# Kernel tuning notes

Hardware: AMD Instinct MI355X
Metric: run time of the kernel (lower is better)

## Reference

```python
import jax, jax.numpy as jnp
import numpy as np

# (C,H,W) of x0..x11; flattened size +1 homogeneous coordinate per key
SHAPES = [(3,32,32),(96,32,32),(96,32,32),(96,16,16),(192,16,16),(192,16,16),(192,8,8),(192,8,8),(192,8,8),(640,1,1),(100,1,1),(10,1,1)]
# (Cin,Cout,k,stride,pad) for conv1..conv9
CONV = [(3,96,3,1,1),(96,96,3,1,1),(96,96,3,2,1),(96,192,3,1,1),(192,192,3,1,1),(192,192,3,2,1),(192,192,3,1,1),(192,192,1,1,0),(192,10,1,1,0)]
B = 128


def setup_inputs():
    key = jax.random.key(0)
    inp = {}
    k, key = jax.random.split(key)
    inp['x0'] = jax.random.normal(k, (int(np.prod(SHAPES[0])) + 1, B), jnp.float32)
    for i, s in enumerate(SHAPES):
        n = int(np.prod(s)) + 1
        k1, k2, key = jax.random.split(key, 3)
        inp['perm%d' % i] = jax.random.permutation(k1, n)
        inp['diag%d' % i] = jax.random.uniform(k2, (n,), jnp.float32, 0.5, 1.5)
    for j, (ci, co, ks, st, pd) in enumerate(CONV):
        k1, k2, key = jax.random.split(key, 3)
        inp['w%d' % (j + 1)] = jax.random.normal(k1, (co, ci, ks, ks), jnp.float32) / np.float32(np.sqrt(ci * ks * ks))
        inp['b%d' % (j + 1)] = jax.random.normal(k2, (co,), jnp.float32) * 0.01
    k1, k2, k3, k4 = jax.random.split(key, 4)
    inp['fw1'] = jax.random.normal(k1, (100, 640), jnp.float32) / np.float32(np.sqrt(640))
    inp['fb1'] = jax.random.normal(k2, (100,), jnp.float32) * 0.01
    inp['fw2'] = jax.random.normal(k3, (10, 100), jnp.float32) / np.float32(np.sqrt(100))
    inp['fb2'] = jax.random.normal(k4, (10,), jnp.float32) * 0.01
    return inp


def _decode(x, perm, diag):
    # A_inv @ x with A_inv = P^T D^{-1}; P^T gather index is argsort(perm)
    return (x / diag[:, None])[jnp.argsort(perm)]


def _encode(y, perm, diag):
    # A @ y with A = D P; (P y)[i] = y[perm[i]]
    return diag[:, None] * y[perm]


def _conv_aug(v, w, b, shape_in, stride, pad):
    # affine-augmented conv: [W b; 0 1] applied to [feat; t]
    C, H, Wd = shape_in
    feat, t = v[:-1], v[-1]                      # (C*H*W, B), (B,)
    x = feat.T.reshape(-1, C, H, Wd)
    y = jax.lax.conv_general_dilated(x, w, (stride, stride), [(pad, pad), (pad, pad)],
                                     dimension_numbers=('NCHW', 'OIHW', 'NCHW'))
    y = y + b[None, :, None, None] * t[:, None, None, None]
    yf = y.reshape(y.shape[0], -1).T             # (N_out, B)
    return jnp.concatenate([yf, t[None, :]], axis=0)


def _fc_aug(v, w, b):
    feat, t = v[:-1], v[-1]
    return jnp.concatenate([w @ feat + b[:, None] * t[None, :], t[None, :]], axis=0)


def _forward(x0, perms, diags, ws, bs, fw1, fb1, fw2, fb2):
    x = x0
    for i in range(9):
        v = _decode(x, perms[i], diags[i])
        y = _conv_aug(v, ws[i], bs[i], SHAPES[i], CONV[i][3], CONV[i][4])
        x = jax.nn.relu(_encode(y, perms[i + 1], diags[i + 1]))
    v = _decode(x, perms[9], diags[9])
    x = jax.nn.relu(_encode(_fc_aug(v, fw1, fb1), perms[10], diags[10]))
    v = _decode(x, perms[10], diags[10])
    return _encode(_fc_aug(v, fw2, fb2), perms[11], diags[11])


def reference(x0, perm0, perm1, perm2, perm3, perm4, perm5, perm6, perm7, perm8, perm9, perm10, perm11,
              diag0, diag1, diag2, diag3, diag4, diag5, diag6, diag7, diag8, diag9, diag10, diag11,
              w1, b1, w2, b2, w3, b3, w4, b4, w5, b5, w6, b6, w7, b7, w8, b8, w9, b9,
              fw1, fb1, fw2, fb2):
    perms = [perm0, perm1, perm2, perm3, perm4, perm5, perm6, perm7, perm8, perm9, perm10, perm11]
    diags = [diag0, diag1, diag2, diag3, diag4, diag5, diag6, diag7, diag8, diag9, diag10, diag11]
    ws = [w1, w2, w3, w4, w5, w6, w7, w8, w9]
    bs = [b1, b2, b3, b4, b5, b6, b7, b8, b9]
    return _forward(x0, perms, diags, ws, bs, fw1, fb1, fw2, fb2)
```

## Files before the change

kernel.cpp:

```cpp
#include <hip/hip_runtime.h>


#define B 128
#define ZPAD 2048

typedef _Float16 f16_t;
typedef __attribute__((ext_vector_type(8))) _Float16 f16x8;
typedef __attribute__((ext_vector_type(4))) _Float16 f16x4;
typedef __attribute__((ext_vector_type(4))) float f32x4;


__global__ void decode_kernel(const float* __restrict__ x, const int* __restrict__ perm,
                              const float* __restrict__ diag, float* __restrict__ v, int nrows) {
    int row = blockIdx.x * 8 + (threadIdx.x >> 5);
    if (row >= nrows) return;
    int lane = threadIdx.x & 31;
    int p = perm[row];
    float inv = 1.0f / diag[row];
    float4 val = ((const float4*)(x + (size_t)row * B))[lane];
    val.x *= inv; val.y *= inv; val.z *= inv; val.w *= inv;
    ((float4*)(v + (size_t)p * B))[lane] = val;
}

__global__ void encode_kernel(const float* __restrict__ y, const int* __restrict__ perm,
                              const float* __restrict__ diag, float* __restrict__ out, int nrows) {
    int row = blockIdx.x * 8 + (threadIdx.x >> 5);
    if (row >= nrows) return;
    int lane = threadIdx.x & 31;
    int p = perm[row];
    float d = diag[row];
    float4 val = ((const float4*)(y + (size_t)p * B))[lane];
    val.x *= d; val.y *= d; val.z *= d; val.w *= d;
    ((float4*)(out + (size_t)row * B))[lane] = val;
}

__global__ void fc_kernel(const float* __restrict__ v, const float* __restrict__ w,
                          const float* __restrict__ b, float* __restrict__ y,
                          int K, int R, int do_relu) {
    int r = blockIdx.x;
    int n = threadIdx.x;
    float t = v[(size_t)K * B + n];
    float val;
    if (r == R) {
        val = t;
    } else {
        float a0 = 0.f, a1 = 0.f, a2 = 0.f, a3 = 0.f;
        float a4 = 0.f, a5 = 0.f, a6 = 0.f, a7 = 0.f;
        const float* wr = w + (size_t)r * K;
        int k = 0;
        for (; k + 8 <= K; k += 8) {
            float4 w0 = *(const float4*)(wr + k);
            float4 w1 = *(const float4*)(wr + k + 4);
            float x0 = v[(size_t)(k + 0) * B + n];
            float x1 = v[(size_t)(k + 1) * B + n];
            float x2 = v[(size_t)(k + 2) * B + n];
            float x3 = v[(size_t)(k + 3) * B + n];
            float x4 = v[(size_t)(k + 4) * B + n];
            float x5 = v[(size_t)(k + 5) * B + n];
            float x6 = v[(size_t)(k + 6) * B + n];
            float x7 = v[(size_t)(k + 7) * B + n];
            a0 = fmaf(w0.x, x0, a0);
            a1 = fmaf(w0.y, x1, a1);
            a2 = fmaf(w0.z, x2, a2);
            a3 = fmaf(w0.w, x3, a3);
            a4 = fmaf(w1.x, x4, a4);
            a5 = fmaf(w1.y, x5, a5);
            a6 = fmaf(w1.z, x6, a6);
            a7 = fmaf(w1.w, x7, a7);
        }
        for (; k < K; ++k)
            a0 = fmaf(wr[k], v[(size_t)k * B + n], a0);
        val = b[r] * t + ((a0 + a1) + (a2 + a3)) + ((a4 + a5) + (a6 + a7));
    }
    if (do_relu) val = fmaxf(val, 0.f);
    y[(size_t)r * B + n] = val;
}


__global__ void pack_input_kernel(const float* __restrict__ v, f16_t* __restrict__ xout,
                                  float* __restrict__ tout) {
    int idx = blockIdx.x * 256 + threadIdx.x;
    int p = idx >> 7, n = idx & 127;
    f16x8 o = {};
    o[0] = (f16_t)v[(size_t)(0 * 1024 + p) * B + n];
    o[1] = (f16_t)v[(size_t)(1 * 1024 + p) * B + n];
    o[2] = (f16_t)v[(size_t)(2 * 1024 + p) * B + n];
    *(f16x8*)(xout + ZPAD + (size_t)p * 1024 + n * 8) = o;
    if (idx < B) tout[idx] = v[(size_t)3072 * B + idx];
}


struct WArgs {
    const float* w[9]; const float* b[9];
    int Ci[9], Co[9], KS[9], Cp[9], NCG[9];
    int woff[10]; int boff[10];
};

__global__ void pack_weights_kernel(WArgs A, f16_t* __restrict__ wp, float* __restrict__ bp,
                                    f16_t* __restrict__ x8a, f16_t* __restrict__ x8b) {
    int idx = blockIdx.x * 256 + threadIdx.x;
    if (idx < ZPAD) { x8a[idx] = (f16_t)0.f; x8b[idx] = (f16_t)0.f; }
    if (idx < A.boff[9]) {
        int l = 0;
        while (idx >= A.boff[l + 1]) ++l;
        int co = idx - A.boff[l];
        bp[idx] = (co < A.Co[l]) ? A.b[l][co] : 0.f;
    }
    if (idx >= A.woff[9]) return;
    int l = 0;
    while (idx >= A.woff[l + 1]) ++l;
    int e = idx - A.woff[l];
    int j = e & 7;
    int t1 = e >> 3;
    int Cp = A.Cp[l];
    int co = t1 % Cp;
    int gg = t1 / Cp;
    int ncg = A.NCG[l];
    int tap = gg / ncg, cg = gg - tap * ncg;
    int ks = A.KS[l];
    int kh = tap / ks, kw = tap - kh * ks;
    int ci = cg * 8 + j;
    float val = 0.f;
    if (co < A.Co[l] && tap < ks * ks && ci < A.Ci[l])
        val = A.w[l][(((size_t)co * A.Ci[l] + ci) * ks + kh) * ks + kw];
    wp[idx] = (f16_t)val;
}


template <int KS, int MS, int NS, int NSPLIT, bool F32OUT>
__global__ __launch_bounds__(256, (MS == 1) ? 3 : 2) void conv_mfma_kernel(
    const f16_t* __restrict__ xin, const float* __restrict__ t_in,
    const f16_t* __restrict__ wp, const float* __restrict__ bp,
    f16_t* __restrict__ xout, float* __restrict__ t_out, float* __restrict__ f32out,
    int Hi, int Wi, int Wo_log2, int HWo,
    int stride, int pad, int NCG, int nchunk, int KGr, int Co, int Co_pad,
    int PB8, int CB)
{
    constexpr int PF = (MS == 1) ? 3 : 2;
    const int wave = threadIdx.x >> 6;
    const int lane = threadIdx.x & 63;
    const int q = lane >> 4;
    const int r = lane & 15;

    const int gb = blockIdx.x;
    const int xcd = gb & 7;
    int j = gb >> 3;
    int nh = 0;
    if (NSPLIT == 2) { nh = j & 1; j >>= 1; }
    const int cog = j % CB;
    const int pb  = xcd * PB8 + j / CB;

    const int p   = (MS == 4) ? (pb * 4 + wave) : pb;
    const int co0 = cog * 64 + ((MS == 1) ? wave * 16 : 0);
    const int ncol0 = nh * (NS * 16);
    const int ncol8 = ncol0 * 8;

    const int ho = p >> Wo_log2;
    const int wo = p & ((1 << Wo_log2) - 1);
    const f16_t* xdata = xin + ZPAD;

    float tv[NS];
#pragma unroll
    for (int ns = 0; ns < NS; ++ns) tv[ns] = t_in[ncol0 + ns * 16 + r];

    f32x4 acc[MS][NS];
#pragma unroll
    for (int ms = 0; ms < MS; ++ms) {
        float4 b4 = *(const float4*)(bp + co0 + ms * 16 + q * 4);
#pragma unroll
        for (int ns = 0; ns < NS; ++ns) {
            acc[ms][ns][0] = b4.x * tv[ns];
            acc[ms][ns][1] = b4.y * tv[ns];
            acc[ms][ns][2] = b4.z * tv[ns];
            acc[ms][ns][3] = b4.w * tv[ns];
        }
    }

    const int hb = ho * stride - pad, wb = wo * stride - pad;
    const int HiWi = Hi * Wi;
    const int HiWi4 = 4 * HiWi;
    const int NCGHW = NCG * HiWi;
    const int wend = wb + KS;

    int g = q, cg = q, hi = hb, wi = wb, cgHW;
    {
        while (cg >= NCG) { cg -= NCG; ++wi; if (wi == wend) { wi = wb; ++hi; } }
        cgHW = cg * HiWi;
    }

    f16x8 bf[PF][NS], af[PF][MS];

    auto advance = [&]() {
        g += 4; cg += 4; cgHW += HiWi4;
        if (NCG >= 4) {
            int c2 = cg - NCG;
            bool wrap = c2 >= 0;
            int wn = wi + 1;
            bool ww = wrap & (wn == wend);
            cg   = wrap ? c2 : cg;
            cgHW = wrap ? cgHW - NCGHW : cgHW;
            wi   = wrap ? (ww ? wb : wn) : wi;
            hi   = ww ? hi + 1 : hi;
        } else {
            while (cg >= NCG) { cg -= NCG; cgHW -= NCGHW; ++wi; if (wi == wend) { wi = wb; ++hi; } }
        }
    };
    auto loadB = [&](f16x8* b) {
        bool v = (g < KGr) & ((unsigned)hi < (unsigned)Hi) & ((unsigned)wi < (unsigned)Wi);
        int boff = (cgHW + hi * Wi + wi) << 10;
        const f16_t* bb = xdata + (v ? boff : -ZPAD) + ncol8 + r * 8;
#pragma unroll
        for (int ns = 0; ns < NS; ++ns) b[ns] = *(const f16x8*)(bb + ns * 128);
    };
    auto loadA = [&](f16x8* a, int c) {
        int ac = c < nchunk ? c : nchunk - 1;
        const f16_t* ap = wp + (((ac * 4 + q) * Co_pad) + co0 + r) * 8;
#pragma unroll
        for (int ms = 0; ms < MS; ++ms) a[ms] = *(const f16x8*)(ap + ms * 128);
    };
    auto domfma = [&](f16x8* a, f16x8* b) {
#pragma unroll
        for (int ms = 0; ms < MS; ++ms)
#pragma unroll
            for (int ns = 0; ns < NS; ++ns)
                acc[ms][ns] = __builtin_amdgcn_mfma_f32_16x16x32_f16(a[ms], b[ns], acc[ms][ns], 0, 0, 0);
    };

#pragma unroll
    for (int pf = 0; pf < PF; ++pf) { loadB(bf[pf]); loadA(af[pf], pf); advance(); }
    const int nck = ((nchunk + PF - 1) / PF) * PF;
    for (int c = 0; c < nck; c += PF) {
#pragma unroll
        for (int pf = 0; pf < PF; ++pf) {
            domfma(af[pf], bf[pf]);
            loadB(bf[pf]); loadA(af[pf], c + PF + pf); advance();
        }
    }

    if (!F32OUT) {
#pragma unroll
        for (int ms = 0; ms < MS; ++ms) {
            int cob = co0 + ms * 16 + q * 4;
            if (cob < Co) {
                int off0 = ((cob >> 3) * HWo + p) * 1024 + (cob & 7) + ncol8 + r * 8;
#pragma unroll
                for (int ns = 0; ns < NS; ++ns) {
                    f16x4 h;
                    h[0] = (f16_t)fmaxf(acc[ms][ns][0], 0.f);
                    h[1] = (f16_t)fmaxf(acc[ms][ns][1], 0.f);
                    h[2] = (f16_t)fmaxf(acc[ms][ns][2], 0.f);
                    h[3] = (f16_t)fmaxf(acc[ms][ns][3], 0.f);
                    *(f16x4*)(xout + ZPAD + off0 + ns * 128) = h;
                }
            }
        }
        if (gb == 0 && threadIdx.x < B)
            t_out[threadIdx.x] = fmaxf(t_in[threadIdx.x], 0.f);
    } else {
#pragma unroll
        for (int ms = 0; ms < MS; ++ms)
#pragma unroll
            for (int ns = 0; ns < NS; ++ns)
#pragma unroll
                for (int e = 0; e < 4; ++e) {
                    int co = co0 + ms * 16 + q * 4 + e;
                    if (co < Co)
                        f32out[((size_t)co * HWo + p) * B + ncol0 + ns * 16 + r] =
                            fmaxf(acc[ms][ns][e], 0.f);
                }
        if (gb == 0 && threadIdx.x < B)
            f32out[(size_t)Co * HWo * B + threadIdx.x] = fmaxf(t_in[threadIdx.x], 0.f);
    }
}


extern "C" void kernel_launch(void* const* d_in, const int* in_sizes, int n_in,
                              void* d_out, int out_size, void* d_ws, size_t ws_size,
                              hipStream_t stream) {
    const float* x0 = (const float*)d_in[0];
    const int*   perm[12];
    const float* diag[12];
    for (int i = 0; i < 12; ++i) {
        perm[i] = (const int*)d_in[1 + 2 * i];
        diag[i] = (const float*)d_in[2 + 2 * i];
    }
    const float* wts[9];
    const float* bia[9];
    for (int j = 0; j < 9; ++j) {
        wts[j] = (const float*)d_in[25 + 2 * j];
        bia[j] = (const float*)d_in[26 + 2 * j];
    }
    const float* fw1 = (const float*)d_in[43];
    const float* fb1 = (const float*)d_in[44];
    const float* fw2 = (const float*)d_in[45];
    const float* fb2 = (const float*)d_in[46];
    float* out = (float*)d_out;

    static const int CiA[9]  = {3, 96, 96, 96, 192, 192, 192, 192, 192};
    static const int CoA[9]  = {96, 96, 96, 192, 192, 192, 192, 192, 10};
    static const int KSA[9]  = {3, 3, 3, 3, 3, 3, 3, 1, 1};
    static const int CpA[9]  = {128, 128, 128, 192, 192, 192, 192, 192, 64};
    static const int NCGA[9] = {1, 12, 12, 12, 24, 24, 24, 24, 24};
    static const int KGRA[9] = {9, 108, 108, 108, 216, 216, 216, 24, 24};
    static const int NCHK[9] = {3, 27, 27, 27, 54, 54, 54, 6, 6};
    static const int HiA[9]  = {32, 32, 32, 16, 16, 16, 8, 8, 8};
    static const int WoL[9]  = {5, 5, 4, 4, 4, 3, 3, 3, 3};
    static const int HWoA[9] = {1024, 1024, 256, 256, 256, 64, 64, 64, 64};
    static const int STA[9]  = {1, 1, 2, 1, 1, 2, 1, 1, 1};
    static const int PDA[9]  = {1, 1, 1, 1, 1, 1, 1, 0, 0};
    static const int MSA[9]  = {4, 4, 1, 1, 1, 1, 1, 1, 1};
    static const int NSPL[9] = {1, 1, 1, 1, 1, 2, 2, 2, 2};

    char* wsb = (char*)d_ws;
    const size_t BUF_F32  = 1574912;
    const size_t X8_BYTES = (size_t)(ZPAD + 12 * 1024 * 1024) * 2;
    float* bufA = (float*)wsb;
    float* bufB = (float*)(wsb + BUF_F32);
    f16_t* x8a  = (f16_t*)(wsb + 2 * BUF_F32);
    f16_t* x8b  = (f16_t*)(wsb + 2 * BUF_F32 + X8_BYTES);
    f16_t* wpb  = (f16_t*)(wsb + 2 * BUF_F32 + 2 * X8_BYTES);
    const size_t WP_BYTES = 2888704;
    float* bpb  = (float*)(wsb + 2 * BUF_F32 + 2 * X8_BYTES + WP_BYTES);
    float* t0   = (float*)((char*)bpb + 8192);
    float* t1   = t0 + 256;

    WArgs WA;
    int wo = 0, bo = 0;
    for (int l = 0; l < 9; ++l) {
        WA.w[l] = wts[l]; WA.b[l] = bia[l];
        WA.Ci[l] = CiA[l]; WA.Co[l] = CoA[l]; WA.KS[l] = KSA[l];
        WA.Cp[l] = CpA[l]; WA.NCG[l] = NCGA[l];
        WA.woff[l] = wo; wo += NCHK[l] * 4 * CpA[l] * 8;
        WA.boff[l] = bo; bo += CpA[l];
    }
    WA.woff[9] = wo; WA.boff[9] = bo;
    pack_weights_kernel<<<(wo + 255) / 256, 256, 0, stream>>>(WA, wpb, bpb, x8a, x8b);

    decode_kernel<<<(3073 + 7) / 8, 256, 0, stream>>>(x0, perm[0], diag[0], bufA, 3073);
    pack_input_kernel<<<131072 / 256, 256, 0, stream>>>(bufA, x8a, t0);

    f16_t* xin = x8a; f16_t* xout = x8b;
    float* tin = t0;  float* tout = t1;
    for (int l = 0; l < 9; ++l) {
        const int ms = MSA[l];
        const int PB = HWoA[l] / (ms == 4 ? 4 : 1);
        const int PB8 = PB / 8;
        const int CB = CpA[l] / 64;
        dim3 grid(8 * PB8 * CB * NSPL[l]);
        const f16_t* wpl = wpb + WA.woff[l];
        const float* bpl = bpb + WA.boff[l];
        if (l <= 1) {
            conv_mfma_kernel<3, 4, 8, 1, false><<<grid, 256, 0, stream>>>(
                xin, tin, wpl, bpl, xout, tout, nullptr,
                HiA[l], HiA[l], WoL[l], HWoA[l], STA[l], PDA[l],
                NCGA[l], NCHK[l], KGRA[l], CoA[l], CpA[l], PB8, CB);
        } else if (l <= 4) {
            conv_mfma_kernel<3, 1, 8, 1, false><<<grid, 256, 0, stream>>>(
                xin, tin, wpl, bpl, xout, tout, nullptr,
                HiA[l], HiA[l], WoL[l], HWoA[l], STA[l], PDA[l],
                NCGA[l], NCHK[l], KGRA[l], CoA[l], CpA[l], PB8, CB);
        } else if (l <= 6) {
            conv_mfma_kernel<3, 1, 4, 2, false><<<grid, 256, 0, stream>>>(
                xin, tin, wpl, bpl, xout, tout, nullptr,
                HiA[l], HiA[l], WoL[l], HWoA[l], STA[l], PDA[l],
                NCGA[l], NCHK[l], KGRA[l], CoA[l], CpA[l], PB8, CB);
        } else if (l == 7) {
            conv_mfma_kernel<1, 1, 4, 2, false><<<grid, 256, 0, stream>>>(
                xin, tin, wpl, bpl, xout, tout, nullptr,
                HiA[l], HiA[l], WoL[l], HWoA[l], STA[l], PDA[l],
                NCGA[l], NCHK[l], KGRA[l], CoA[l], CpA[l], PB8, CB);
        } else {
            conv_mfma_kernel<1, 1, 4, 2, true><<<grid, 256, 0, stream>>>(
                xin, tin, wpl, bpl, nullptr, nullptr, bufA,
                HiA[l], HiA[l], WoL[l], HWoA[l], STA[l], PDA[l],
                NCGA[l], NCHK[l], KGRA[l], CoA[l], CpA[l], PB8, CB);
        }
        f16_t* xt = xin; xin = xout; xout = xt;
        float* tt = tin; tin = tout; tout = tt;
    }

    fc_kernel<<<101, B, 0, stream>>>(bufA, fw1, fb1, bufB, 640, 100, 1);
    fc_kernel<<<11, B, 0, stream>>>(bufB, fw2, fb2, bufA, 100, 10, 0);
    encode_kernel<<<2, 256, 0, stream>>>(bufA, perm[11], diag[11], out, 11);
}
```

Baseline: 374.3 us.

## Switch conv kernel to single-wave blocks each computing a full 64-channel tile

```diff
diff --git a/kernel.cpp b/kernel.cpp
--- a/kernel.cpp
+++ b/kernel.cpp
@@ -127,8 +127,8 @@
 }
 
 
-template <int KS, int MS, int NS, int NSPLIT, bool F32OUT>
-__global__ __launch_bounds__(256, (MS == 1) ? 3 : 2) void conv_mfma_kernel(
+template <int KS, int NS, int NSPLIT, bool F32OUT>
+__global__ __launch_bounds__(64) void conv_mfma_kernel(
     const f16_t* __restrict__ xin, const float* __restrict__ t_in,
     const f16_t* __restrict__ wp, const float* __restrict__ bp,
     f16_t* __restrict__ xout, float* __restrict__ t_out, float* __restrict__ f32out,
@@ -136,9 +136,9 @@
     int stride, int pad, int NCG, int nchunk, int KGr, int Co, int Co_pad,
     int PB8, int CB)
 {
-    constexpr int PF = (MS == 1) ? 3 : 2;
-    const int wave = threadIdx.x >> 6;
-    const int lane = threadIdx.x & 63;
+    constexpr int PF = 2;
+    constexpr int MS = 4;
+    const int lane = threadIdx.x;
     const int q = lane >> 4;
     const int r = lane & 15;
 
@@ -148,10 +148,8 @@
     int nh = 0;
     if (NSPLIT == 2) { nh = j & 1; j >>= 1; }
     const int cog = j % CB;
-    const int pb  = xcd * PB8 + j / CB;
-
-    const int p   = (MS == 4) ? (pb * 4 + wave) : pb;
-    const int co0 = cog * 64 + ((MS == 1) ? wave * 16 : 0);
+    const int p   = xcd * PB8 + j / CB;
+    const int co0 = cog * 64;
     const int ncol0 = nh * (NS * 16);
     const int ncol8 = ncol0 * 8;
 
@@ -254,8 +252,10 @@
                 }
             }
         }
-        if (gb == 0 && threadIdx.x < B)
-            t_out[threadIdx.x] = fmaxf(t_in[threadIdx.x], 0.f);
+        if (gb == 0) {
+            t_out[lane]      = fmaxf(t_in[lane], 0.f);
+            t_out[lane + 64] = fmaxf(t_in[lane + 64], 0.f);
+        }
     } else {
 #pragma unroll
         for (int ms = 0; ms < MS; ++ms)
@@ -268,8 +268,10 @@
                         f32out[((size_t)co * HWo + p) * B + ncol0 + ns * 16 + r] =
                             fmaxf(acc[ms][ns][e], 0.f);
                 }
-        if (gb == 0 && threadIdx.x < B)
-            f32out[(size_t)Co * HWo * B + threadIdx.x] = fmaxf(t_in[threadIdx.x], 0.f);
+        if (gb == 0) {
+            f32out[(size_t)Co * HWo * B + lane]      = fmaxf(t_in[lane], 0.f);
+            f32out[(size_t)Co * HWo * B + lane + 64] = fmaxf(t_in[lane + 64], 0.f);
+        }
     }
 }
 
@@ -308,7 +310,6 @@
     static const int HWoA[9] = {1024, 1024, 256, 256, 256, 64, 64, 64, 64};
     static const int STA[9]  = {1, 1, 2, 1, 1, 2, 1, 1, 1};
     static const int PDA[9]  = {1, 1, 1, 1, 1, 1, 1, 0, 0};
-    static const int MSA[9]  = {4, 4, 1, 1, 1, 1, 1, 1, 1};
     static const int NSPL[9] = {1, 1, 1, 1, 1, 2, 2, 2, 2};
 
     char* wsb = (char*)d_ws;
@@ -342,35 +343,28 @@
     f16_t* xin = x8a; f16_t* xout = x8b;
     float* tin = t0;  float* tout = t1;
     for (int l = 0; l < 9; ++l) {
-        const int ms = MSA[l];
-        const int PB = HWoA[l] / (ms == 4 ? 4 : 1);
-        const int PB8 = PB / 8;
+        const int PB8 = HWoA[l] / 8;
         const int CB = CpA[l] / 64;
         dim3 grid(8 * PB8 * CB * NSPL[l]);
         const f16_t* wpl = wpb + WA.woff[l];
         const float* bpl = bpb + WA.boff[l];
-        if (l <= 1) {
-            conv_mfma_kernel<3, 4, 8, 1, false><<<grid, 256, 0, stream>>>(
-                xin, tin, wpl, bpl, xout, tout, nullptr,
-                HiA[l], HiA[l], WoL[l], HWoA[l], STA[l], PDA[l],
-                NCGA[l], NCHK[l], KGRA[l], CoA[l], CpA[l], PB8, CB);
-        } else if (l <= 4) {
-            conv_mfma_kernel<3, 1, 8, 1, false><<<grid, 256, 0, stream>>>(
+        if (l <= 4) {
+            conv_mfma_kernel<3, 8, 1, false><<<grid, 64, 0, stream>>>(
                 xin, tin, wpl, bpl, xout, tout, nullptr,
                 HiA[l], HiA[l], WoL[l], HWoA[l], STA[l], PDA[l],
                 NCGA[l], NCHK[l], KGRA[l], CoA[l], CpA[l], PB8, CB);
         } else if (l <= 6) {
-            conv_mfma_kernel<3, 1, 4, 2, false><<<grid, 256, 0, stream>>>(
+            conv_mfma_kernel<3, 4, 2, false><<<grid, 64, 0, stream>>>(
                 xin, tin, wpl, bpl, xout, tout, nullptr,
                 HiA[l], HiA[l], WoL[l], HWoA[l], STA[l], PDA[l],
                 NCGA[l], NCHK[l], KGRA[l], CoA[l], CpA[l], PB8, CB);
         } else if (l == 7) {
-            conv_mfma_kernel<1, 1, 4, 2, false><<<grid, 256, 0, stream>>>(
+            conv_mfma_kernel<1, 4, 2, false><<<grid, 64, 0, stream>>>(
                 xin, tin, wpl, bpl, xout, tout, nullptr,
                 HiA[l], HiA[l], WoL[l], HWoA[l], STA[l], PDA[l],
                 NCGA[l], NCHK[l], KGRA[l], CoA[l], CpA[l], PB8, CB);
         } else {
-            conv_mfma_kernel<1, 1, 4, 2, true><<<grid, 256, 0, stream>>>(
+            conv_mfma_kernel<1, 4, 2, true><<<grid, 64, 0, stream>>>(
                 xin, tin, wpl, bpl, nullptr, nullptr, bufA,
                 HiA[l], HiA[l], WoL[l], HWoA[l], STA[l], PDA[l],
                 NCGA[l], NCHK[l], KGRA[l], CoA[l], CpA[l], PB8, CB);
```

Result: faster. 336.5 us (-10.1%).
